# Kernel optimization log

Measured on AMD Instinct MI355X. Metric: run time of the kernel, lower is better.

Reference implementation:

```python
import math
import jax, jax.numpy as jnp
import numpy as np

B, N, C = 2, 2048, 1024
H = 16
D = C // H  # 64
LN_EPS = 1e-5


def setup_inputs() -> dict:
    key = jax.random.key(0)
    ks = jax.random.split(key, 5)
    x = jax.random.normal(ks[0], (B, N, C), dtype=jnp.float32)
    w_qkv = jax.random.normal(ks[1], (C, 3 * C), dtype=jnp.float32) * 0.02
    w_proj = jax.random.normal(ks[2], (C, C), dtype=jnp.float32) * 0.02
    b_proj = jnp.zeros((C,), dtype=jnp.float32)
    ln_w = jnp.ones((D,), dtype=jnp.float32) + jax.random.normal(ks[3], (D,), dtype=jnp.float32) * 0.02
    ln_b = jax.random.normal(ks[4], (D,), dtype=jnp.float32) * 0.02
    return {"x": x, "w_qkv": w_qkv, "w_proj": w_proj, "b_proj": b_proj,
            "ln_w": ln_w, "ln_b": ln_b}


def _layernorm(t, w, b):
    mu = jnp.mean(t, axis=-1, keepdims=True)
    var = jnp.var(t, axis=-1, keepdims=True)
    return (t - mu) * jax.lax.rsqrt(var + LN_EPS) * w + b


def reference(x, w_qkv, w_proj, b_proj, ln_w, ln_b):
    b, n, c = x.shape
    h, d = H, c // H
    # QKV projection (no bias): [b,n,3c] -> [3,b,h,n,d]
    qkv = (x @ w_qkv).reshape(b, n, 3, h, d).transpose(2, 0, 3, 1, 4)
    q, k, v = qkv[0], qkv[1], qkv[2]
    # per-head LayerNorm on q and k (qk_norm)
    q = _layernorm(q, ln_w, ln_b)
    k = _layernorm(k, ln_w, ln_b)
    # NOTE: source multiplies q by sqrt(head_dim) (faithful to original)
    q = q * jnp.asarray(math.sqrt(d), dtype=q.dtype)
    scores = jnp.einsum('bhnd,bhmd->bhnm', q, k)  # [b,h,n,n]
    mask_value = -jnp.finfo(scores.dtype).max
    causal = jnp.tril(jnp.ones((n, n), dtype=bool))
    scores = jnp.where(causal, scores, mask_value)
    attn = jax.nn.softmax(scores, axis=-1)
    out = jnp.einsum('bhnm,bhmd->bhnd', attn, v)  # [b,h,n,d]
    out = out.transpose(0, 2, 1, 3).reshape(b, n, c)  # b n (h d)
    return out @ w_proj + b_proj
```

## Files before the change

### kernel.cpp

```cpp
#include <hip/hip_runtime.h>

#define LOG2E 1.4426950408889634f

typedef _Float16 f16x8_t __attribute__((ext_vector_type(8)));
typedef _Float16 f16x4_t __attribute__((ext_vector_type(4)));
typedef _Float16 f16x2_t __attribute__((ext_vector_type(2)));
typedef float    f32x4_t __attribute__((ext_vector_type(4)));

#define MFMA32(a, b, c) __builtin_amdgcn_mfma_f32_16x16x32_f16(a, b, c, 0, 0, 0)
#define MFMA16(a, b, c) __builtin_amdgcn_mfma_f32_16x16x16f16(a, b, c, 0, 0, 0)

__device__ __forceinline__ void async_copy16(void* lds, const void* g) {
    __builtin_amdgcn_global_load_lds(
        (const __attribute__((address_space(1))) unsigned char*)g,
        (__attribute__((address_space(3))) unsigned char*)lds, 16, 0, 0);
}

__global__ void cast_f32_f16_k(const float* __restrict__ in, _Float16* __restrict__ out, int n4) {
    int i = blockIdx.x * blockDim.x + threadIdx.x;
    if (i >= n4) return;
    float4 v = ((const float4*)in)[i];
    f16x4_t o = { (_Float16)v.x, (_Float16)v.y, (_Float16)v.z, (_Float16)v.w };
    ((f16x4_t*)out)[i] = o;
}

__global__ void transpose_cast_k(const float* __restrict__ in, _Float16* __restrict__ out,
                                 int R, int C) {
    __shared__ _Float16 tl[64][65];
    const int t = threadIdx.x;
    const int c = t & 63;
    const int r4 = t >> 6;
    const int r0 = blockIdx.y * 64, c0 = blockIdx.x * 64;
#pragma unroll
    for (int i = 0; i < 16; ++i) {
        int r = r4 + i * 4;
        tl[c][r] = (_Float16)in[(size_t)(r0 + r) * C + c0 + c];
    }
    __syncthreads();
#pragma unroll
    for (int i = 0; i < 16; ++i) {
        int rr = r4 + i * 4;
        out[(size_t)(c0 + rr) * R + r0 + c] = tl[rr][c];
    }
}

__global__ void vtrans_k(const _Float16* __restrict__ qkv, _Float16* __restrict__ VTg) {
    __shared__ _Float16 tl[64][68];
    const int tid = threadIdx.x;
    const int bh = blockIdx.x;
    const int b = bh >> 4, h = bh & 15;
    const int t = blockIdx.y;
    const int c = tid & 63;
    const int r4 = tid >> 6;
#pragma unroll
    for (int i = 0; i < 16; ++i) {
        int r = r4 + i * 4;
        tl[c][r] = qkv[(size_t)(b * 2048 + t * 64 + r) * 3072 + 2048 + h * 64 + c];
    }
    __syncthreads();
    const size_t obase = (size_t)bh * 131072 + (size_t)t * 4096;
#pragma unroll
    for (int e = 0; e < 2; ++e) {
        const int ci = tid * 2 + e;
        const int d = ci >> 3, w = ci & 7;
        const int pq = w ^ (d & 7);
        const int base = (pq >> 2) * 32 + (pq & 3) * 4;
        f16x4_t v0 = *(const f16x4_t*)&tl[d][base];
        f16x4_t v1 = *(const f16x4_t*)&tl[d][base + 16];
        f16x8_t val = __builtin_shufflevector(v0, v1, 0, 1, 2, 3, 4, 5, 6, 7);
        *(f16x8_t*)&VTg[obase + ci * 8] = val;
    }
}

template <typename OutT, bool BIAS>
__global__ __launch_bounds__(256, 3)
void gemm_f16_k(const _Float16* __restrict__ A, const _Float16* __restrict__ BT,
                OutT* __restrict__ C, const float* __restrict__ bias,
                int M, int N, int K) {
    __shared__ _Float16 As[2][128][32];
    __shared__ _Float16 Bs[2][128][32];
    const int tid = threadIdx.x;
    const int wid = tid >> 6, lane = tid & 63;
    const int qd = lane >> 4, ln = lane & 15;
    const int m0 = blockIdx.x * 128, n0 = blockIdx.y * 128;
    const int wm = (wid >> 1) * 64, wn = (wid & 1) * 64;

    f32x4_t acc[4][4] = {};

    const int srow = lane >> 2;
    const int skk  = (lane & 3) * 8;

    for (int k0 = 0; k0 < K; k0 += 64) {
        __syncthreads();
#pragma unroll
        for (int p = 0; p < 4; ++p) {
            const int seg = p * 4 + wid;
            const int s   = seg >> 3;
            const int rg  = seg & 7;
            const int row = rg * 16 + srow;
            const size_t goff = (size_t)row * K + k0 + s * 32 + skk;
            async_copy16(&As[0][0][0] + seg * 512, A  + (size_t)m0 * K + goff);
            async_copy16(&Bs[0][0][0] + seg * 512, BT + (size_t)n0 * K + goff);
        }
        __syncthreads();
#pragma unroll
        for (int s = 0; s < 2; ++s) {
            f16x8_t a[4], b[4];
#pragma unroll
            for (int i = 0; i < 4; ++i)
                a[i] = *(const f16x8_t*)&As[s][wm + i * 16 + ln][qd * 8];
#pragma unroll
            for (int j = 0; j < 4; ++j)
                b[j] = *(const f16x8_t*)&Bs[s][wn + j * 16 + ln][qd * 8];
#pragma unroll
            for (int i = 0; i < 4; ++i)
#pragma unroll
                for (int j = 0; j < 4; ++j)
                    acc[i][j] = MFMA32(a[i], b[j], acc[i][j]);
        }
    }
#pragma unroll
    for (int i = 0; i < 4; ++i)
#pragma unroll
        for (int j = 0; j < 4; ++j) {
            const int col = n0 + wn + j * 16 + ln;
            const float bv = BIAS ? bias[col] : 0.0f;
#pragma unroll
            for (int r = 0; r < 4; ++r) {
                const int row = m0 + wm + i * 16 + qd * 4 + r;
                C[(size_t)row * N + col] = (OutT)(acc[i][j][r] + bv);
            }
        }
}

__global__ __launch_bounds__(256, 2)
void gemm_f16_m64_k(const _Float16* __restrict__ A, const _Float16* __restrict__ BT,
                    float* __restrict__ C, const float* __restrict__ bias,
                    int M, int N, int K) {
    __shared__ _Float16 As[2][64][32];
    __shared__ _Float16 Bs[2][128][32];
    const int tid = threadIdx.x;
    const int wid = tid >> 6, lane = tid & 63;
    const int qd = lane >> 4, ln = lane & 15;
    const int m0 = blockIdx.x * 64, n0 = blockIdx.y * 128;
    const int wn = wid * 32;

    f32x4_t acc[4][2] = {};
    const int srow = lane >> 2;
    const int skk  = (lane & 3) * 8;

    for (int k0 = 0; k0 < K; k0 += 64) {
        __syncthreads();
#pragma unroll
        for (int p = 0; p < 2; ++p) {
            const int seg = p * 4 + wid;
            const int hidx = seg * 512 + lane * 8;
            const int s_ = hidx >> 11;
            const int row = (hidx >> 5) & 63;
            const int kk = hidx & 31;
            async_copy16(&As[0][0][0] + seg * 512,
                         A + (size_t)(m0 + row) * K + k0 + s_ * 32 + kk);
        }
#pragma unroll
        for (int p = 0; p < 4; ++p) {
            const int seg = p * 4 + wid;
            const int s   = seg >> 3;
            const int rg  = seg & 7;
            const int row = rg * 16 + srow;
            async_copy16(&Bs[0][0][0] + seg * 512,
                         BT + (size_t)(n0 + row) * K + k0 + s * 32 + skk);
        }
        __syncthreads();
#pragma unroll
        for (int s = 0; s < 2; ++s) {
            f16x8_t a[4], b[2];
#pragma unroll
            for (int i = 0; i < 4; ++i)
                a[i] = *(const f16x8_t*)&As[s][i * 16 + ln][qd * 8];
#pragma unroll
            for (int j = 0; j < 2; ++j)
                b[j] = *(const f16x8_t*)&Bs[s][wn + j * 16 + ln][qd * 8];
#pragma unroll
            for (int i = 0; i < 4; ++i)
#pragma unroll
                for (int j = 0; j < 2; ++j)
                    acc[i][j] = MFMA32(a[i], b[j], acc[i][j]);
        }
    }
#pragma unroll
    for (int i = 0; i < 4; ++i)
#pragma unroll
        for (int j = 0; j < 2; ++j) {
            const int col = n0 + wn + j * 16 + ln;
            const float bv = bias[col];
#pragma unroll
            for (int r = 0; r < 4; ++r) {
                const int row = m0 + i * 16 + qd * 4 + r;
                C[(size_t)row * N + col] = acc[i][j][r] + bv;
            }
        }
}

__global__ void ln_qk_k(const _Float16* __restrict__ qkv, const float* __restrict__ ln_w,
                        const float* __restrict__ ln_b, _Float16* __restrict__ Qb,
                        _Float16* __restrict__ Kb) {
    const int tid = threadIdx.x;
    const int wid = tid >> 6, lane = tid & 63;
    const int row = blockIdx.x * 4 + wid;
    const int t = row >> 4;
    const int h = row & 15;
    const int b = t >> 11, n = t & 2047;
    const size_t base = (size_t)t * 3072 + h * 64 + lane;
    float q = (float)qkv[base];
    float k = (float)qkv[base + 1024];
    const float wv = ln_w[lane], bv = ln_b[lane];

    float sq = q, sk = k;
#pragma unroll
    for (int m = 1; m < 64; m <<= 1) { sq += __shfl_xor(sq, m); sk += __shfl_xor(sk, m); }
    sq *= (1.0f / 64.0f); sk *= (1.0f / 64.0f);
    const float dq = q - sq, dk = k - sk;
    float vq = dq * dq, vk = dk * dk;
#pragma unroll
    for (int m = 1; m < 64; m <<= 1) { vq += __shfl_xor(vq, m); vk += __shfl_xor(vk, m); }
    vq *= (1.0f / 64.0f); vk *= (1.0f / 64.0f);
    const float yq = dq * rsqrtf(vq + 1e-5f) * wv + bv;
    const float yk = dk * rsqrtf(vk + 1e-5f) * wv + bv;
    const size_t obase = ((size_t)((b * 16 + h) * 2048 + n)) * 64 + lane;
    Qb[obase] = (_Float16)(yq * (8.0f * LOG2E));
    Kb[obase] = (_Float16)yk;
}

__global__ __launch_bounds__(256, 3)
void attn_part_k(const _Float16* __restrict__ Q, const _Float16* __restrict__ K,
                 const _Float16* __restrict__ VTg, _Float16* __restrict__ O,
                 float* __restrict__ Op, float* __restrict__ ml) {
    __shared__ _Float16 Ks[2][2][64][32];
    __shared__ _Float16 VT[2][64][64];

    const int tid = threadIdx.x;
    const int wid = tid >> 6, lane = tid & 63;
    const int qd = lane >> 4, ln = lane & 15;
    const int bh = blockIdx.x;
    const int b = bh >> 4, h = bh & 15;
    const int y = blockIdx.y;
    int band, chunk, nst;
    if (y < 16)      { band = 16 + y; chunk = 0; nst = 16; }
    else if (y < 32) { band = 47 - y; chunk = 1; nst = band - 15; }
    else             { band = 47 - y; chunk = 0; nst = band + 1; }
    const size_t kvbase = (size_t)bh * 2048 * 64;
    const size_t vtbase = (size_t)bh * 131072;
    const int qrow0 = band * 64 + wid * 16;
    const int kvbeg = chunk * 1024;

    f16x8_t qf[2];
#pragma unroll
    for (int s = 0; s < 2; ++s)
        qf[s] = *(const f16x8_t*)&Q[kvbase + (size_t)(qrow0 + ln) * 64 + s * 32 + qd * 8];

    f32x4_t o[4] = {};
    float m = -3.0e38f, l = 0.0f;

    auto stage = [&](int buf, int kv0) {
#pragma unroll
        for (int p = 0; p < 2; ++p) {
            const int seg = p * 4 + wid;
            const int hidx = seg * 512 + lane * 8;
            const int s_ = hidx >> 11;
            const int rrow = (hidx >> 5) & 63;
            const int kk = hidx & 31;
            async_copy16(&Ks[buf][0][0][0] + seg * 512,
                         K + kvbase + (size_t)(kv0 + rrow) * 64 + s_ * 32 + kk);
        }
#pragma unroll
        for (int p = 0; p < 2; ++p) {
            const int seg = p * 4 + wid;
            async_copy16(&VT[buf][0][0] + seg * 512,
                         VTg + vtbase + (size_t)kv0 * 64 + seg * 512 + lane * 8);
        }
    };

    stage(0, kvbeg);

    for (int st = 0; st < nst; ++st) {
        const int kv0 = kvbeg + st * 64;
        __syncthreads();
        if (st + 1 < nst) stage((st + 1) & 1, kv0 + 64);
        const int buf = st & 1;

        f16x8_t kb[4][2];
#pragma unroll
        for (int jt = 0; jt < 4; ++jt)
#pragma unroll
            for (int s = 0; s < 2; ++s)
                kb[jt][s] = *(const f16x8_t*)&Ks[buf][s][jt * 16 + ln][qd * 8];
        f16x8_t vf8[4][2];
#pragma unroll
        for (int dt = 0; dt < 4; ++dt)
#pragma unroll
            for (int pp = 0; pp < 2; ++pp) {
                const int w = (pp * 4 + qd) ^ (ln & 7);
                vf8[dt][pp] = *(const f16x8_t*)&VT[buf][dt * 16 + ln][w * 8];
            }

        f32x4_t sc[4];
#pragma unroll
        for (int jt = 0; jt < 4; ++jt) {
            f32x4_t s = {};
            s = MFMA32(kb[jt][0], qf[0], s);
            s = MFMA32(kb[jt][1], qf[1], s);
            sc[jt] = s;
        }
        if (kv0 + 63 > qrow0) {
            const int qq = qrow0 + ln;
#pragma unroll
            for (int c = 0; c < 4; ++c)
#pragma unroll
                for (int r = 0; r < 4; ++r)
                    if (kv0 + c * 16 + qd * 4 + r > qq) sc[c][r] = -3.0e38f;
        }
        float mx = sc[0][0];
#pragma unroll
        for (int c = 0; c < 4; ++c)
#pragma unroll
            for (int r = 0; r < 4; ++r) mx = fmaxf(mx, sc[c][r]);
        mx = fmaxf(mx, __shfl_xor(mx, 16));
        mx = fmaxf(mx, __shfl_xor(mx, 32));
        const float mn = fmaxf(m, mx);
        const float al = exp2f(m - mn);
        m = mn;
        float rs = 0.0f;
        f16x4_t pf[4];
#pragma unroll
        for (int c = 0; c < 4; ++c) {
            float p0 = exp2f(sc[c][0] - mn);
            float p1 = exp2f(sc[c][1] - mn);
            float p2 = exp2f(sc[c][2] - mn);
            float p3 = exp2f(sc[c][3] - mn);
            rs += (p0 + p1) + (p2 + p3);
            f16x2_t a = __builtin_bit_cast(f16x2_t, __builtin_amdgcn_cvt_pkrtz(p0, p1));
            f16x2_t bb = __builtin_bit_cast(f16x2_t, __builtin_amdgcn_cvt_pkrtz(p2, p3));
            pf[c] = __builtin_shufflevector(a, bb, 0, 1, 2, 3);
        }
        l = l * al + rs;
#pragma unroll
        for (int dt = 0; dt < 4; ++dt) o[dt] *= al;
#pragma unroll
        for (int dt = 0; dt < 4; ++dt)
#pragma unroll
            for (int pp = 0; pp < 2; ++pp) {
                f16x4_t lo = __builtin_shufflevector(vf8[dt][pp], vf8[dt][pp], 0, 1, 2, 3);
                f16x4_t hi = __builtin_shufflevector(vf8[dt][pp], vf8[dt][pp], 4, 5, 6, 7);
                o[dt] = MFMA16(lo, pf[pp * 2 + 0], o[dt]);
                o[dt] = MFMA16(hi, pf[pp * 2 + 1], o[dt]);
            }
    }

    float lt = l + __shfl_xor(l, 16);
    lt = lt + __shfl_xor(lt, 32);

    if (band < 16) {
        const float inv = 1.0f / lt;
        const size_t base = ((size_t)(b * 2048 + qrow0 + ln)) * 1024 + h * 64 + qd * 4;
#pragma unroll
        for (int dt = 0; dt < 4; ++dt) {
            f16x4_t ov;
#pragma unroll
            for (int r = 0; r < 4; ++r) ov[r] = (_Float16)(o[dt][r] * inv);
            *(f16x4_t*)&O[base + dt * 16] = ov;
        }
    } else {
        const size_t pb = (((size_t)bh * 16 + (band - 16)) * 2 + chunk);
        const int row = wid * 16 + ln;
        float* op = Op + pb * 4096 + (size_t)row * 64 + qd * 4;
#pragma unroll
        for (int dt = 0; dt < 4; ++dt)
            *(f32x4_t*)&op[dt * 16] = o[dt];
        if (qd == 0) {
            ml[pb * 128 + row * 2]     = m;
            ml[pb * 128 + row * 2 + 1] = lt;
        }
    }
}

__global__ __launch_bounds__(256)
void attn_merge_k(const float* __restrict__ Op, const float* __restrict__ ml,
                  _Float16* __restrict__ O) {
    const int bh = blockIdx.x, bnd = blockIdx.y;
    const int b = bh >> 4, h = bh & 15;
    const int band = 16 + bnd;
    const size_t pb = ((size_t)bh * 16 + bnd) * 2;
    const int tid = threadIdx.x;
    const int row = tid >> 2;
    const int c4 = (tid & 3) * 16;
    const float m0 = ml[pb * 128 + row * 2],     l0 = ml[pb * 128 + row * 2 + 1];
    const float m1 = ml[pb * 128 + 128 + row * 2], l1 = ml[pb * 128 + 128 + row * 2 + 1];
    const float mm = fmaxf(m0, m1);
    const float a0 = exp2f(m0 - mm), a1 = exp2f(m1 - mm);
    const float inv = 1.0f / (l0 * a0 + l1 * a1);
    const float* p0 = Op + pb * 4096 + (size_t)row * 64 + c4;
    const float* p1 = p0 + 4096;
    _Float16* op = O + ((size_t)(b * 2048 + band * 64 + row)) * 1024 + h * 64 + c4;
#pragma unroll
    for (int g = 0; g < 4; ++g) {
        f32x4_t v0 = *(const f32x4_t*)&p0[g * 4];
        f32x4_t v1 = *(const f32x4_t*)&p1[g * 4];
        f16x4_t ov;
#pragma unroll
        for (int r = 0; r < 4; ++r)
            ov[r] = (_Float16)((v0[r] * a0 + v1[r] * a1) * inv);
        *(f16x4_t*)&op[g * 4] = ov;
    }
}

extern "C" void kernel_launch(void* const* d_in, const int* in_sizes, int n_in,
                              void* d_out, int out_size, void* d_ws, size_t ws_size,
                              hipStream_t stream) {
    const float* x      = (const float*)d_in[0];
    const float* w_qkv  = (const float*)d_in[1];
    const float* w_proj = (const float*)d_in[2];
    const float* b_proj = (const float*)d_in[3];
    const float* ln_w   = (const float*)d_in[4];
    const float* ln_b   = (const float*)d_in[5];
    float* out = (float*)d_out;

    char* w = (char*)d_ws;
    _Float16*  qkv    = (_Float16*)w;  w += (size_t)4096 * 3072 * 2;
    _Float16*  xh     = (_Float16*)w;  w += (size_t)4096 * 1024 * 2;
    _Float16*  wqkvT  = (_Float16*)w;  w += (size_t)3072 * 1024 * 2;
    _Float16*  wprojT = (_Float16*)w;  w += (size_t)1024 * 1024 * 2;
    _Float16*  Qb     = (_Float16*)w;  w += (size_t)32 * 2048 * 64 * 2;
    _Float16*  Kb     = (_Float16*)w;  w += (size_t)32 * 2048 * 64 * 2;
    _Float16*  VTg    = (_Float16*)w;  w += (size_t)32 * 64 * 2048 * 2;
    _Float16*  Ah     = (_Float16*)w;  w += (size_t)4096 * 1024 * 2;
    float*     Op     = (float*)w;     w += (size_t)32 * 16 * 2 * 4096 * 4;
    float*     mlb    = (float*)w;     w += (size_t)32 * 16 * 2 * 128 * 4;

    cast_f32_f16_k<<<4096, 256, 0, stream>>>(x, xh, 4096 * 1024 / 4);
    transpose_cast_k<<<dim3(48, 16), 256, 0, stream>>>(w_qkv, wqkvT, 1024, 3072);
    transpose_cast_k<<<dim3(16, 16), 256, 0, stream>>>(w_proj, wprojT, 1024, 1024);
    gemm_f16_k<_Float16, false><<<dim3(32, 24), 256, 0, stream>>>(xh, wqkvT, qkv, nullptr, 4096, 3072, 1024);
    vtrans_k<<<dim3(32, 32), 256, 0, stream>>>(qkv, VTg);
    ln_qk_k<<<16384, 256, 0, stream>>>(qkv, ln_w, ln_b, Qb, Kb);
    attn_part_k<<<dim3(32, 48), 256, 0, stream>>>(Qb, Kb, VTg, Ah, Op, mlb);
    attn_merge_k<<<dim3(32, 16), 256, 0, stream>>>(Op, mlb, Ah);
    gemm_f16_m64_k<<<dim3(64, 8), 256, 0, stream>>>(Ah, wprojT, out, b_proj, 4096, 1024, 1024);
}
```

Before: 208.1 us.

## Process 128-row query bands per block with two q-tiles per wave

The attention kernel now gives each block 128 query rows (32 per wave as two 16-row tiles), so each K/V tile staged in LDS is reused across twice as many queries. The grid shrinks to 24 band/chunk slots and the merge kernel is adjusted to match. Two further changes ride along: the row sum is accumulated with an MFMA against a ones vector instead of scalar adds, and the running max is only rescaled when it rises by more than 8 in log2 units (lazy rescale). The trade-offs are higher register pressure per wave and fewer blocks in flight, which lowers occupancy. Fully masked tiles for a wave are also skipped.

```diff
diff --git a/kernel.cpp b/kernel.cpp
--- a/kernel.cpp
+++ b/kernel.cpp
@@ -245,21 +245,25 @@
     const int b = bh >> 4, h = bh & 15;
     const int y = blockIdx.y;
     int band, chunk, nst;
-    if (y < 16)      { band = 16 + y; chunk = 0; nst = 16; }
-    else if (y < 32) { band = 47 - y; chunk = 1; nst = band - 15; }
-    else             { band = 47 - y; chunk = 0; nst = band + 1; }
+    if (y < 8)       { band = 8 + y;  chunk = 0; nst = 16; }
+    else if (y < 16) { band = 23 - y; chunk = 1; nst = 2 * band - 14; }
+    else             { band = y - 16; chunk = 0; nst = 2 * band + 2; }
     const size_t kvbase = (size_t)bh * 2048 * 64;
     const size_t vtbase = (size_t)bh * 131072;
-    const int qrow0 = band * 64 + wid * 16;
+    const int qrow0 = band * 128 + wid * 32;
     const int kvbeg = chunk * 1024;
 
-    f16x8_t qf[2];
-#pragma unroll
-    for (int s = 0; s < 2; ++s)
-        qf[s] = *(const f16x8_t*)&Q[kvbase + (size_t)(qrow0 + ln) * 64 + s * 32 + qd * 8];
-
-    f32x4_t o[4] = {};
-    float m = -3.0e38f, l = 0.0f;
+    f16x8_t qf[2][2];
+#pragma unroll
+    for (int qt = 0; qt < 2; ++qt)
+#pragma unroll
+        for (int s = 0; s < 2; ++s)
+            qf[qt][s] = *(const f16x8_t*)&Q[kvbase + (size_t)(qrow0 + qt * 16 + ln) * 64 + s * 32 + qd * 8];
+
+    f32x4_t o[2][4] = {};
+    f32x4_t ls[2] = {};
+    float m[2] = { -3.0e38f, -3.0e38f };
+    const f16x4_t ones = { (_Float16)1.0f, (_Float16)1.0f, (_Float16)1.0f, (_Float16)1.0f };
 
     auto stage = [&](int buf, int kv0) {
 #pragma unroll
@@ -288,97 +292,108 @@
         if (st + 1 < nst) stage((st + 1) & 1, kv0 + 64);
         const int buf = st & 1;
 
-        f16x8_t kb[4][2];
-#pragma unroll
-        for (int jt = 0; jt < 4; ++jt)
-#pragma unroll
-            for (int s = 0; s < 2; ++s)
-                kb[jt][s] = *(const f16x8_t*)&Ks[buf][s][jt * 16 + ln][qd * 8];
-        f16x8_t vf8[4][2];
-#pragma unroll
-        for (int dt = 0; dt < 4; ++dt)
-#pragma unroll
-            for (int pp = 0; pp < 2; ++pp) {
-                const int w = (pp * 4 + qd) ^ (ln & 7);
-                vf8[dt][pp] = *(const f16x8_t*)&VT[buf][dt * 16 + ln][w * 8];
-            }
-
-        f32x4_t sc[4];
-#pragma unroll
-        for (int jt = 0; jt < 4; ++jt) {
-            f32x4_t s = {};
-            s = MFMA32(kb[jt][0], qf[0], s);
-            s = MFMA32(kb[jt][1], qf[1], s);
-            sc[jt] = s;
-        }
-        if (kv0 + 63 > qrow0) {
-            const int qq = qrow0 + ln;
-#pragma unroll
-            for (int c = 0; c < 4; ++c)
-#pragma unroll
-                for (int r = 0; r < 4; ++r)
-                    if (kv0 + c * 16 + qd * 4 + r > qq) sc[c][r] = -3.0e38f;
-        }
-        float mx = sc[0][0];
-#pragma unroll
-        for (int c = 0; c < 4; ++c)
-#pragma unroll
-            for (int r = 0; r < 4; ++r) mx = fmaxf(mx, sc[c][r]);
-        mx = fmaxf(mx, __shfl_xor(mx, 16));
-        mx = fmaxf(mx, __shfl_xor(mx, 32));
-        const float mn = fmaxf(m, mx);
-        const float al = exp2f(m - mn);
-        m = mn;
-        float rs = 0.0f;
-        f16x4_t pf[4];
-#pragma unroll
-        for (int c = 0; c < 4; ++c) {
-            float p0 = exp2f(sc[c][0] - mn);
-            float p1 = exp2f(sc[c][1] - mn);
-            float p2 = exp2f(sc[c][2] - mn);
-            float p3 = exp2f(sc[c][3] - mn);
-            rs += (p0 + p1) + (p2 + p3);
-            f16x2_t a = __builtin_bit_cast(f16x2_t, __builtin_amdgcn_cvt_pkrtz(p0, p1));
-            f16x2_t bb = __builtin_bit_cast(f16x2_t, __builtin_amdgcn_cvt_pkrtz(p2, p3));
-            pf[c] = __builtin_shufflevector(a, bb, 0, 1, 2, 3);
-        }
-        l = l * al + rs;
-#pragma unroll
-        for (int dt = 0; dt < 4; ++dt) o[dt] *= al;
-#pragma unroll
-        for (int dt = 0; dt < 4; ++dt)
-#pragma unroll
-            for (int pp = 0; pp < 2; ++pp) {
-                f16x4_t lo = __builtin_shufflevector(vf8[dt][pp], vf8[dt][pp], 0, 1, 2, 3);
-                f16x4_t hi = __builtin_shufflevector(vf8[dt][pp], vf8[dt][pp], 4, 5, 6, 7);
-                o[dt] = MFMA16(lo, pf[pp * 2 + 0], o[dt]);
-                o[dt] = MFMA16(hi, pf[pp * 2 + 1], o[dt]);
-            }
-    }
-
-    float lt = l + __shfl_xor(l, 16);
-    lt = lt + __shfl_xor(lt, 32);
-
-    if (band < 16) {
-        const float inv = 1.0f / lt;
-        const size_t base = ((size_t)(b * 2048 + qrow0 + ln)) * 1024 + h * 64 + qd * 4;
-#pragma unroll
-        for (int dt = 0; dt < 4; ++dt) {
-            f16x4_t ov;
-#pragma unroll
-            for (int r = 0; r < 4; ++r) ov[r] = (_Float16)(o[dt][r] * inv);
-            *(f16x4_t*)&O[base + dt * 16] = ov;
+        if (kv0 <= qrow0 + 31) {
+            f32x4_t sc[2][4];
+#pragma unroll
+            for (int jt = 0; jt < 4; ++jt) {
+                f16x8_t k0 = *(const f16x8_t*)&Ks[buf][0][jt * 16 + ln][qd * 8];
+                f16x8_t k1 = *(const f16x8_t*)&Ks[buf][1][jt * 16 + ln][qd * 8];
+#pragma unroll
+                for (int qt = 0; qt < 2; ++qt) {
+                    f32x4_t s = {};
+                    s = MFMA32(k0, qf[qt][0], s);
+                    s = MFMA32(k1, qf[qt][1], s);
+                    sc[qt][jt] = s;
+                }
+            }
+            f16x8_t vf8[4][2];
+#pragma unroll
+            for (int dt = 0; dt < 4; ++dt)
+#pragma unroll
+                for (int pp = 0; pp < 2; ++pp) {
+                    const int w = (pp * 4 + qd) ^ (ln & 7);
+                    vf8[dt][pp] = *(const f16x8_t*)&VT[buf][dt * 16 + ln][w * 8];
+                }
+
+#pragma unroll
+            for (int qt = 0; qt < 2; ++qt) {
+                if (kv0 + 63 > qrow0 + qt * 16) {
+                    const int qq = qrow0 + qt * 16 + ln;
+#pragma unroll
+                    for (int c = 0; c < 4; ++c)
+#pragma unroll
+                        for (int r = 0; r < 4; ++r)
+                            if (kv0 + c * 16 + qd * 4 + r > qq) sc[qt][c][r] = -3.0e38f;
+                }
+                f32x4_t mq = sc[qt][0];
+#pragma unroll
+                for (int c = 1; c < 4; ++c)
+#pragma unroll
+                    for (int r = 0; r < 4; ++r) mq[r] = fmaxf(mq[r], sc[qt][c][r]);
+                float mx = fmaxf(fmaxf(mq[0], mq[1]), fmaxf(mq[2], mq[3]));
+                mx = fmaxf(mx, __shfl_xor(mx, 16));
+                mx = fmaxf(mx, __shfl_xor(mx, 32));
+                if (!__all(mx <= m[qt] + 8.0f)) {
+                    const float mn = fmaxf(m[qt], mx);
+                    const float al = exp2f(m[qt] - mn);
+#pragma unroll
+                    for (int dt = 0; dt < 4; ++dt) o[qt][dt] *= al;
+                    ls[qt][0] *= al;
+                    m[qt] = mn;
+                }
+                f16x4_t pf[4];
+#pragma unroll
+                for (int c = 0; c < 4; ++c) {
+                    float p0 = exp2f(sc[qt][c][0] - m[qt]);
+                    float p1 = exp2f(sc[qt][c][1] - m[qt]);
+                    float p2 = exp2f(sc[qt][c][2] - m[qt]);
+                    float p3 = exp2f(sc[qt][c][3] - m[qt]);
+                    f16x2_t a = __builtin_bit_cast(f16x2_t, __builtin_amdgcn_cvt_pkrtz(p0, p1));
+                    f16x2_t bb = __builtin_bit_cast(f16x2_t, __builtin_amdgcn_cvt_pkrtz(p2, p3));
+                    pf[c] = __builtin_shufflevector(a, bb, 0, 1, 2, 3);
+                }
+#pragma unroll
+                for (int c = 0; c < 4; ++c) ls[qt] = MFMA16(ones, pf[c], ls[qt]);
+#pragma unroll
+                for (int dt = 0; dt < 4; ++dt)
+#pragma unroll
+                    for (int pp = 0; pp < 2; ++pp) {
+                        f16x4_t lo = __builtin_shufflevector(vf8[dt][pp], vf8[dt][pp], 0, 1, 2, 3);
+                        f16x4_t hi = __builtin_shufflevector(vf8[dt][pp], vf8[dt][pp], 4, 5, 6, 7);
+                        o[qt][dt] = MFMA16(lo, pf[pp * 2 + 0], o[qt][dt]);
+                        o[qt][dt] = MFMA16(hi, pf[pp * 2 + 1], o[qt][dt]);
+                    }
+            }
+        }
+    }
+
+    if (band < 8) {
+        const size_t base0 = ((size_t)(b * 2048 + qrow0 + ln)) * 1024 + h * 64 + qd * 4;
+#pragma unroll
+        for (int qt = 0; qt < 2; ++qt) {
+            const float inv = 1.0f / ls[qt][0];
+            const size_t base = base0 + (size_t)qt * 16 * 1024;
+#pragma unroll
+            for (int dt = 0; dt < 4; ++dt) {
+                f16x4_t ov;
+#pragma unroll
+                for (int r = 0; r < 4; ++r) ov[r] = (_Float16)(o[qt][dt][r] * inv);
+                *(f16x4_t*)&O[base + dt * 16] = ov;
+            }
         }
     } else {
-        const size_t pb = (((size_t)bh * 16 + (band - 16)) * 2 + chunk);
-        const int row = wid * 16 + ln;
-        float* op = Op + pb * 4096 + (size_t)row * 64 + qd * 4;
-#pragma unroll
-        for (int dt = 0; dt < 4; ++dt)
-            *(f32x4_t*)&op[dt * 16] = o[dt];
-        if (qd == 0) {
-            ml[pb * 128 + row * 2]     = m;
-            ml[pb * 128 + row * 2 + 1] = lt;
+        const size_t pb = ((size_t)bh * 8 + (band - 8)) * 2 + chunk;
+#pragma unroll
+        for (int qt = 0; qt < 2; ++qt) {
+            const int row = wid * 32 + qt * 16 + ln;
+            float* op = Op + pb * 8192 + (size_t)row * 64 + qd * 4;
+#pragma unroll
+            for (int dt = 0; dt < 4; ++dt)
+                *(f32x4_t*)&op[dt * 16] = o[qt][dt];
+            if (qd == 0) {
+                ml[pb * 256 + row * 2]     = m[qt];
+                ml[pb * 256 + row * 2 + 1] = ls[qt][0];
+            }
         }
     }
 }
@@ -388,21 +403,21 @@
                   _Float16* __restrict__ O) {
     const int bh = blockIdx.x, bnd = blockIdx.y;
     const int b = bh >> 4, h = bh & 15;
-    const int band = 16 + bnd;
-    const size_t pb = ((size_t)bh * 16 + bnd) * 2;
-    const int tid = threadIdx.x;
-    const int row = tid >> 2;
-    const int c4 = (tid & 3) * 16;
-    const float m0 = ml[pb * 128 + row * 2],     l0 = ml[pb * 128 + row * 2 + 1];
-    const float m1 = ml[pb * 128 + 128 + row * 2], l1 = ml[pb * 128 + 128 + row * 2 + 1];
+    const int band = 8 + bnd;
+    const size_t pb = ((size_t)bh * 8 + bnd) * 2;
+    const int tid = threadIdx.x;
+    const int row = tid >> 1;
+    const int c32 = (tid & 1) * 32;
+    const float m0 = ml[pb * 256 + row * 2],       l0 = ml[pb * 256 + row * 2 + 1];
+    const float m1 = ml[(pb + 1) * 256 + row * 2], l1 = ml[(pb + 1) * 256 + row * 2 + 1];
     const float mm = fmaxf(m0, m1);
     const float a0 = exp2f(m0 - mm), a1 = exp2f(m1 - mm);
     const float inv = 1.0f / (l0 * a0 + l1 * a1);
-    const float* p0 = Op + pb * 4096 + (size_t)row * 64 + c4;
-    const float* p1 = p0 + 4096;
-    _Float16* op = O + ((size_t)(b * 2048 + band * 64 + row)) * 1024 + h * 64 + c4;
-#pragma unroll
-    for (int g = 0; g < 4; ++g) {
+    const float* p0 = Op + pb * 8192 + (size_t)row * 64 + c32;
+    const float* p1 = p0 + 8192;
+    _Float16* op = O + ((size_t)(b * 2048 + band * 128 + row)) * 1024 + h * 64 + c32;
+#pragma unroll
+    for (int g = 0; g < 8; ++g) {
         f32x4_t v0 = *(const f32x4_t*)&p0[g * 4];
         f32x4_t v1 = *(const f32x4_t*)&p1[g * 4];
         f16x4_t ov;
@@ -433,8 +448,8 @@
     _Float16*  Kb     = (_Float16*)w;  w += (size_t)32 * 2048 * 64 * 2;
     _Float16*  VTg    = (_Float16*)w;  w += (size_t)32 * 64 * 2048 * 2;
     _Float16*  Ah     = (_Float16*)w;  w += (size_t)4096 * 1024 * 2;
-    float*     Op     = (float*)w;     w += (size_t)32 * 16 * 2 * 4096 * 4;
-    float*     mlb    = (float*)w;     w += (size_t)32 * 16 * 2 * 128 * 4;
+    float*     Op     = (float*)w;     w += (size_t)32 * 8 * 2 * 8192 * 4;
+    float*     mlb    = (float*)w;     w += (size_t)32 * 8 * 2 * 256 * 4;
 
     cast_f32_f16_k<<<4096, 256, 0, stream>>>(x, xh, 4096 * 1024 / 4);
     transpose_cast_k<<<dim3(48, 16), 256, 0, stream>>>(w_qkv, wqkvT, 1024, 3072);
@@ -442,7 +457,7 @@
     gemm_f16_k<_Float16, false><<<dim3(32, 24), 256, 0, stream>>>(xh, wqkvT, qkv, nullptr, 4096, 3072, 1024);
     vtrans_k<<<dim3(32, 32), 256, 0, stream>>>(qkv, VTg);
     ln_qk_k<<<16384, 256, 0, stream>>>(qkv, ln_w, ln_b, Qb, Kb);
-    attn_part_k<<<dim3(32, 48), 256, 0, stream>>>(Qb, Kb, VTg, Ah, Op, mlb);
-    attn_merge_k<<<dim3(32, 16), 256, 0, stream>>>(Op, mlb, Ah);
+    attn_part_k<<<dim3(32, 24), 256, 0, stream>>>(Qb, Kb, VTg, Ah, Op, mlb);
+    attn_merge_k<<<dim3(32, 8), 256, 0, stream>>>(Op, mlb, Ah);
     gemm_f16_m64_k<<<dim3(64, 8), 256, 0, stream>>>(Ah, wprojT, out, b_proj, 4096, 1024, 1024);
 }
```

Measured after the change: 213.6 us. 1.03x slower.
